# Performance work log

Measured on AMD Instinct MI355X. Metric: run time of the kernel, lower is better.

Reference implementation:

```python
import jax, jax.numpy as jnp
import numpy as np

N = 100000
E = 3200000
CONV = 16
HID = 1024
OUT = 256
NEG_SLOPE = 0.01  # torch leaky_relu default


def leaky_relu(x):
    return jnp.where(x >= 0, x, NEG_SLOPE * x)


def gcn_conv(x, W, b, src, dst, n):
    # PyG GCNConv: add self-loops, symmetric norm, linear, scatter-add, bias
    loop = jnp.arange(n)
    s = jnp.concatenate([src, loop])
    d = jnp.concatenate([dst, loop])
    deg = jax.ops.segment_sum(jnp.ones_like(d, dtype=x.dtype), d, num_segments=n)
    dinv = jnp.where(deg > 0, jax.lax.rsqrt(deg), 0.0)
    norm = dinv[s] * dinv[d]                      # [E+N]
    h = x @ W                                     # [N, out_ch]
    msg = h[s] * norm[:, None]                    # gather + scale
    out = jax.ops.segment_sum(msg, d, num_segments=n)  # scatter-add
    return out + b


def setup_inputs() -> dict:
    key = jax.random.key(0)
    ks = jax.random.split(key, 10)
    return {
        "x": jax.random.normal(ks[0], (N, 1), dtype=jnp.float32),
        "edge_index": jax.random.randint(ks[1], (2, E), 0, N, dtype=jnp.int64),
        "W1c": jax.random.normal(ks[2], (1, CONV), dtype=jnp.float32) * 0.5,
        "b1c": jnp.zeros((CONV,), dtype=jnp.float32),
        "W2c": jax.random.normal(ks[3], (CONV, 1), dtype=jnp.float32) * 0.25,
        "b2c": jnp.zeros((1,), dtype=jnp.float32),
        "Wf1": jax.random.normal(ks[4], (HID, N), dtype=jnp.float32) * 0.003,
        "bf1": jnp.zeros((HID,), dtype=jnp.float32),
        "Wf2": jax.random.normal(ks[5], (OUT, HID), dtype=jnp.float32) * 0.03,
        "bf2": jnp.zeros((OUT,), dtype=jnp.float32),
    }


def reference(x, edge_index, W1c, b1c, W2c, b2c, Wf1, bf1, Wf2, bf2):
    src, dst = edge_index[0], edge_index[1]
    h = gcn_conv(x, W1c, b1c, src, dst, N)        # [N, CONV]
    h = leaky_relu(h)
    h = gcn_conv(h, W2c, b2c, src, dst, N)        # [N, 1]
    h = leaky_relu(h)
    v = h.T.squeeze()                             # [N]
    z = leaky_relu(Wf1 @ v + bf1)                 # [HID]
    z = Wf2 @ z + bf2                             # [OUT]
    return jax.nn.log_softmax(z, axis=0)
```

## Files before the change

### kernel.cpp

```cpp
#include <hip/hip_runtime.h>
#include <math.h>


constexpr int NN    = 100000;
constexpr int NE    = 3200000;
constexpr int CONVC = 16;
constexpr int HID   = 1024;
constexpr int NOUT  = 256;
constexpr int PART  = 128;
constexpr int P     = (NN + PART - 1) / PART;
constexpr int CAP   = 5120;
constexpr int SB    = 256;
constexpr int EPB   = NE / SB;
#define NEG 0.01f

__device__ __forceinline__ float lrelu(float x) { return x >= 0.0f ? x : NEG * x; }

__device__ __forceinline__ float wave_reduce_sum(float v) {
#pragma unroll
  for (int off = 32; off > 0; off >>= 1) v += __shfl_down(v, off, 64);
  return v;
}

__global__ __launch_bounds__(256) void k_init(int* __restrict__ gcur) {
  int i = blockIdx.x * 256 + threadIdx.x;
  if (i < P) gcur[i] = i * CAP;
}

__global__ __launch_bounds__(1024) void k_bucket(const int* __restrict__ src,
                                                 const int* __restrict__ dst,
                                                 int* __restrict__ gcur,
                                                 int* __restrict__ packed) {
  __shared__ int hist[P];
  __shared__ int lcur[P];
  int t = threadIdx.x;
  for (int b = t; b < P; b += 1024) hist[b] = 0;
  __syncthreads();
  int base = blockIdx.x * EPB;
  int lim = min(EPB, NE - base);
  for (int e = t; e < lim; e += 1024) atomicAdd(&hist[dst[base + e] >> 7], 1);
  __syncthreads();
  for (int b = t; b < P; b += 1024) lcur[b] = atomicAdd(&gcur[b], hist[b]);
  __syncthreads();
  for (int e = t; e < lim; e += 1024) {
    int d = dst[base + e];
    int s = src[base + e];
    int pos = atomicAdd(&lcur[d >> 7], 1);
    packed[pos] = ((d & 127) << 17) | s;
  }
}

__global__ __launch_bounds__(256) void k_bin_deg(const int* __restrict__ packed,
                                                 const int* __restrict__ gcur,
                                                 const float* __restrict__ x,
                                                 float* __restrict__ dinv,
                                                 float* __restrict__ xs) {
  __shared__ float acc[PART];
  int p = blockIdx.x, t = threadIdx.x;
  if (t < PART) acc[t] = 0.0f;
  __syncthreads();
  int beg = p * CAP, end = gcur[p];
  for (int i = beg + t; i < end; i += 256) atomicAdd(&acc[packed[i] >> 17], 1.0f);
  __syncthreads();
  int j = p * PART + t;
  if (t < PART && j < NN) {
    float di = rsqrtf(acc[t] + 1.0f);
    dinv[j] = di;
    xs[j] = x[j] * di;
  }
}

__global__ __launch_bounds__(256) void k_bin_s1(const int* __restrict__ packed,
                                                const int* __restrict__ gcur,
                                                const float* __restrict__ val,
                                                const float* __restrict__ x,
                                                const float* __restrict__ dinv,
                                                const float* __restrict__ W1,
                                                const float* __restrict__ b1,
                                                const float* __restrict__ W2,
                                                float* __restrict__ qv,
                                                float* __restrict__ xs2) {
  __shared__ float acc[PART];
  int p = blockIdx.x, t = threadIdx.x;
  if (t < PART) acc[t] = 0.0f;
  __syncthreads();
  int beg = p * CAP, end = gcur[p];
  for (int i = beg + t; i < end; i += 256) {
    int pk = packed[i];
    atomicAdd(&acc[pk >> 17], val[pk & 0x1FFFF]);
  }
  __syncthreads();
  int j = p * PART + t;
  if (t < PART && j < NN) {
    float di = dinv[j];
    float pv = di * (acc[t] + x[j] * di);
    float q = 0.0f;
#pragma unroll
    for (int ch = 0; ch < CONVC; ch++) q += lrelu(pv * W1[ch] + b1[ch]) * W2[ch];
    qv[j] = q;
    xs2[j] = q * di;
  }
}

__global__ __launch_bounds__(256) void k_bin_s2(const int* __restrict__ packed,
                                                const int* __restrict__ gcur,
                                                const float* __restrict__ val,
                                                const float* __restrict__ qv,
                                                const float* __restrict__ dinv,
                                                const float* __restrict__ b2c,
                                                float* __restrict__ v) {
  __shared__ float acc[PART];
  int p = blockIdx.x, t = threadIdx.x;
  if (t < PART) acc[t] = 0.0f;
  __syncthreads();
  int beg = p * CAP, end = gcur[p];
  for (int i = beg + t; i < end; i += 256) {
    int pk = packed[i];
    atomicAdd(&acc[pk >> 17], val[pk & 0x1FFFF]);
  }
  __syncthreads();
  int j = p * PART + t;
  if (t < PART && j < NN) {
    float di = dinv[j];
    float r = di * (acc[t] + qv[j] * di) + b2c[0];
    v[j] = lrelu(r);
  }
}

__global__ __launch_bounds__(256) void k_mv1(const float* __restrict__ Wf1,
                                             const float* __restrict__ v,
                                             const float* __restrict__ bf1,
                                             float* __restrict__ z) {
  int row = blockIdx.x;
  const float4* w4 = reinterpret_cast<const float4*>(Wf1 + (size_t)row * NN);
  const float4* v4 = reinterpret_cast<const float4*>(v);
  float sum = 0.0f;
  for (int j = threadIdx.x; j < NN / 4; j += 256) {
    float4 w = w4[j];
    float4 vv = v4[j];
    sum += w.x * vv.x + w.y * vv.y + w.z * vv.z + w.w * vv.w;
  }
  sum = wave_reduce_sum(sum);
  __shared__ float ss[4];
  if ((threadIdx.x & 63) == 0) ss[threadIdx.x >> 6] = sum;
  __syncthreads();
  if (threadIdx.x == 0) z[row] = lrelu(ss[0] + ss[1] + ss[2] + ss[3] + bf1[row]);
}

__global__ __launch_bounds__(256) void k_mv2(const float* __restrict__ Wf2,
                                             const float* __restrict__ z,
                                             const float* __restrict__ bf2,
                                             float* __restrict__ tmp) {
  int o = blockIdx.x;
  const float4* w4 = reinterpret_cast<const float4*>(Wf2 + (size_t)o * HID);
  const float4* z4 = reinterpret_cast<const float4*>(z);
  int j = threadIdx.x;
  float4 w = w4[j];
  float4 zv = z4[j];
  float sum = w.x * zv.x + w.y * zv.y + w.z * zv.z + w.w * zv.w;
  sum = wave_reduce_sum(sum);
  __shared__ float ss[4];
  if ((threadIdx.x & 63) == 0) ss[threadIdx.x >> 6] = sum;
  __syncthreads();
  if (threadIdx.x == 0) tmp[o] = ss[0] + ss[1] + ss[2] + ss[3] + bf2[o];
}

__global__ __launch_bounds__(256) void k_lsm(const float* __restrict__ tmp,
                                             float* __restrict__ out) {
  int t = threadIdx.x;
  float vv = tmp[t];
  __shared__ float buf[256];
  buf[t] = vv;
  __syncthreads();
  for (int s = 128; s > 0; s >>= 1) {
    if (t < s) buf[t] = fmaxf(buf[t], buf[t + s]);
    __syncthreads();
  }
  float m = buf[0];
  __syncthreads();
  buf[t] = expf(vv - m);
  __syncthreads();
  for (int s = 128; s > 0; s >>= 1) {
    if (t < s) buf[t] += buf[t + s];
    __syncthreads();
  }
  float lse = logf(buf[0]);
  out[t] = vv - m - lse;
}

extern "C" void kernel_launch(void* const* d_in, const int* in_sizes, int n_in,
                              void* d_out, int out_size, void* d_ws, size_t ws_size,
                              hipStream_t stream) {
  const float* x   = (const float*)d_in[0];
  const int*   ei  = (const int*)d_in[1];
  const float* W1c = (const float*)d_in[2];
  const float* b1c = (const float*)d_in[3];
  const float* W2c = (const float*)d_in[4];
  const float* b2c = (const float*)d_in[5];
  const float* Wf1 = (const float*)d_in[6];
  const float* bf1 = (const float*)d_in[7];
  const float* Wf2 = (const float*)d_in[8];
  const float* bf2 = (const float*)d_in[9];
  float* out = (float*)d_out;

  const int* src = ei;
  const int* dst = ei + NE;

  float* ws   = (float*)d_ws;
  float* dinv = ws;
  float* xs   = dinv + NN;
  float* qv   = xs + NN;
  float* xs2  = qv + NN;
  float* v    = xs2 + NN;
  float* z    = v + NN;
  float* tmp  = z + HID;
  int*   gcur   = (int*)(tmp + NOUT);
  int*   packed = gcur + P;

  k_init<<<(P + 255) / 256, 256, 0, stream>>>(gcur);
  k_bucket<<<SB, 1024, 0, stream>>>(src, dst, gcur, packed);
  k_bin_deg<<<P, 256, 0, stream>>>(packed, gcur, x, dinv, xs);
  k_bin_s1<<<P, 256, 0, stream>>>(packed, gcur, xs, x, dinv, W1c, b1c, W2c, qv, xs2);
  k_bin_s2<<<P, 256, 0, stream>>>(packed, gcur, xs2, qv, dinv, b2c, v);
  k_mv1<<<HID, 256, 0, stream>>>(Wf1, v, bf1, z);
  k_mv2<<<NOUT, 256, 0, stream>>>(Wf2, z, bf2, tmp);
  k_lsm<<<1, 256, 0, stream>>>(tmp, out);
}
```

Baseline: 686.4 us.

## Widen bins to 256 nodes, vectorize edge loads, split shared accumulators

Bucket partitions grow from 128 to 256 destination nodes, which halves the number of bins and makes every thread in the 256-thread block own an output row. The bucketing kernel reads src and dst as int4 and keeps dst in registers between the histogram pass and the scatter pass, so dst is read from global memory only once. The per-bin kernels read packed entries as int4 and spread the shared-memory atomics over two accumulator copies to cut contention. The workspace is reordered so packed starts at the base and stays 16-byte aligned. The risks are fixed-capacity bins (CAP) that could overflow on other graphs, and more register pressure from holding dst in registers.

```diff
diff --git a/kernel.cpp b/kernel.cpp
--- a/kernel.cpp
+++ b/kernel.cpp
@@ -7,11 +7,13 @@
 constexpr int CONVC = 16;
 constexpr int HID   = 1024;
 constexpr int NOUT  = 256;
-constexpr int PART  = 128;
+constexpr int PART  = 256;
 constexpr int P     = (NN + PART - 1) / PART;
-constexpr int CAP   = 5120;
+constexpr int CAP   = 9472;
 constexpr int SB    = 256;
-constexpr int EPB   = NE / SB;
+constexpr int NE4   = NE / 4;
+constexpr int EPB4  = NE4 / SB;
+constexpr int RPT   = (EPB4 + 1023) / 1024;
 #define NEG 0.01f
 
 __device__ __forceinline__ float lrelu(float x) { return x >= 0.0f ? x : NEG * x; }
@@ -27,8 +29,8 @@
   if (i < P) gcur[i] = i * CAP;
 }
 
-__global__ __launch_bounds__(1024) void k_bucket(const int* __restrict__ src,
-                                                 const int* __restrict__ dst,
+__global__ __launch_bounds__(1024) void k_bucket(const int4* __restrict__ src4,
+                                                 const int4* __restrict__ dst4,
                                                  int* __restrict__ gcur,
                                                  int* __restrict__ packed) {
   __shared__ int hist[P];
@@ -36,17 +38,32 @@
   int t = threadIdx.x;
   for (int b = t; b < P; b += 1024) hist[b] = 0;
   __syncthreads();
-  int base = blockIdx.x * EPB;
-  int lim = min(EPB, NE - base);
-  for (int e = t; e < lim; e += 1024) atomicAdd(&hist[dst[base + e] >> 7], 1);
+  int base4 = blockIdx.x * EPB4;
+  int4 dreg[RPT];
+#pragma unroll
+  for (int k = 0; k < RPT; k++) {
+    if (t + k * 1024 < EPB4) {
+      int4 d = dst4[base4 + t + k * 1024];
+      dreg[k] = d;
+      atomicAdd(&hist[d.x >> 8], 1);
+      atomicAdd(&hist[d.y >> 8], 1);
+      atomicAdd(&hist[d.z >> 8], 1);
+      atomicAdd(&hist[d.w >> 8], 1);
+    }
+  }
   __syncthreads();
   for (int b = t; b < P; b += 1024) lcur[b] = atomicAdd(&gcur[b], hist[b]);
   __syncthreads();
-  for (int e = t; e < lim; e += 1024) {
-    int d = dst[base + e];
-    int s = src[base + e];
-    int pos = atomicAdd(&lcur[d >> 7], 1);
-    packed[pos] = ((d & 127) << 17) | s;
+#pragma unroll
+  for (int k = 0; k < RPT; k++) {
+    if (t + k * 1024 < EPB4) {
+      int4 s = src4[base4 + t + k * 1024];
+      int4 d = dreg[k];
+      int p0 = atomicAdd(&lcur[d.x >> 8], 1); packed[p0] = ((d.x & 255) << 17) | s.x;
+      int p1 = atomicAdd(&lcur[d.y >> 8], 1); packed[p1] = ((d.y & 255) << 17) | s.y;
+      int p2 = atomicAdd(&lcur[d.z >> 8], 1); packed[p2] = ((d.z & 255) << 17) | s.z;
+      int p3 = atomicAdd(&lcur[d.w >> 8], 1); packed[p3] = ((d.w & 255) << 17) | s.w;
+    }
   }
 }
 
@@ -55,16 +72,27 @@
                                                  const float* __restrict__ x,
                                                  float* __restrict__ dinv,
                                                  float* __restrict__ xs) {
-  __shared__ float acc[PART];
+  __shared__ float acc[2][PART];
   int p = blockIdx.x, t = threadIdx.x;
-  if (t < PART) acc[t] = 0.0f;
-  __syncthreads();
+  acc[0][t] = 0.0f;
+  acc[1][t] = 0.0f;
+  __syncthreads();
+  float* myacc = acc[t >> 7];
   int beg = p * CAP, end = gcur[p];
-  for (int i = beg + t; i < end; i += 256) atomicAdd(&acc[packed[i] >> 17], 1.0f);
+  int n = end - beg, n4 = n >> 2;
+  const int4* pk4 = reinterpret_cast<const int4*>(packed + beg);
+  for (int i = t; i < n4; i += 256) {
+    int4 e = pk4[i];
+    atomicAdd(&myacc[e.x >> 17], 1.0f);
+    atomicAdd(&myacc[e.y >> 17], 1.0f);
+    atomicAdd(&myacc[e.z >> 17], 1.0f);
+    atomicAdd(&myacc[e.w >> 17], 1.0f);
+  }
+  for (int i = (n4 << 2) + t; i < n; i += 256) atomicAdd(&myacc[packed[beg + i] >> 17], 1.0f);
   __syncthreads();
   int j = p * PART + t;
-  if (t < PART && j < NN) {
-    float di = rsqrtf(acc[t] + 1.0f);
+  if (j < NN) {
+    float di = rsqrtf(acc[0][t] + acc[1][t] + 1.0f);
     dinv[j] = di;
     xs[j] = x[j] * di;
   }
@@ -80,20 +108,31 @@
                                                 const float* __restrict__ W2,
                                                 float* __restrict__ qv,
                                                 float* __restrict__ xs2) {
-  __shared__ float acc[PART];
+  __shared__ float acc[2][PART];
   int p = blockIdx.x, t = threadIdx.x;
-  if (t < PART) acc[t] = 0.0f;
-  __syncthreads();
+  acc[0][t] = 0.0f;
+  acc[1][t] = 0.0f;
+  __syncthreads();
+  float* myacc = acc[t >> 7];
   int beg = p * CAP, end = gcur[p];
-  for (int i = beg + t; i < end; i += 256) {
-    int pk = packed[i];
-    atomicAdd(&acc[pk >> 17], val[pk & 0x1FFFF]);
+  int n = end - beg, n4 = n >> 2;
+  const int4* pk4 = reinterpret_cast<const int4*>(packed + beg);
+  for (int i = t; i < n4; i += 256) {
+    int4 e = pk4[i];
+    atomicAdd(&myacc[e.x >> 17], val[e.x & 0x1FFFF]);
+    atomicAdd(&myacc[e.y >> 17], val[e.y & 0x1FFFF]);
+    atomicAdd(&myacc[e.z >> 17], val[e.z & 0x1FFFF]);
+    atomicAdd(&myacc[e.w >> 17], val[e.w & 0x1FFFF]);
+  }
+  for (int i = (n4 << 2) + t; i < n; i += 256) {
+    int pk = packed[beg + i];
+    atomicAdd(&myacc[pk >> 17], val[pk & 0x1FFFF]);
   }
   __syncthreads();
   int j = p * PART + t;
-  if (t < PART && j < NN) {
+  if (j < NN) {
     float di = dinv[j];
-    float pv = di * (acc[t] + x[j] * di);
+    float pv = di * (acc[0][t] + acc[1][t] + x[j] * di);
     float q = 0.0f;
 #pragma unroll
     for (int ch = 0; ch < CONVC; ch++) q += lrelu(pv * W1[ch] + b1[ch]) * W2[ch];
@@ -109,20 +148,31 @@
                                                 const float* __restrict__ dinv,
                                                 const float* __restrict__ b2c,
                                                 float* __restrict__ v) {
-  __shared__ float acc[PART];
+  __shared__ float acc[2][PART];
   int p = blockIdx.x, t = threadIdx.x;
-  if (t < PART) acc[t] = 0.0f;
-  __syncthreads();
+  acc[0][t] = 0.0f;
+  acc[1][t] = 0.0f;
+  __syncthreads();
+  float* myacc = acc[t >> 7];
   int beg = p * CAP, end = gcur[p];
-  for (int i = beg + t; i < end; i += 256) {
-    int pk = packed[i];
-    atomicAdd(&acc[pk >> 17], val[pk & 0x1FFFF]);
+  int n = end - beg, n4 = n >> 2;
+  const int4* pk4 = reinterpret_cast<const int4*>(packed + beg);
+  for (int i = t; i < n4; i += 256) {
+    int4 e = pk4[i];
+    atomicAdd(&myacc[e.x >> 17], val[e.x & 0x1FFFF]);
+    atomicAdd(&myacc[e.y >> 17], val[e.y & 0x1FFFF]);
+    atomicAdd(&myacc[e.z >> 17], val[e.z & 0x1FFFF]);
+    atomicAdd(&myacc[e.w >> 17], val[e.w & 0x1FFFF]);
+  }
+  for (int i = (n4 << 2) + t; i < n; i += 256) {
+    int pk = packed[beg + i];
+    atomicAdd(&myacc[pk >> 17], val[pk & 0x1FFFF]);
   }
   __syncthreads();
   int j = p * PART + t;
-  if (t < PART && j < NN) {
+  if (j < NN) {
     float di = dinv[j];
-    float r = di * (acc[t] + qv[j] * di) + b2c[0];
+    float r = di * (acc[0][t] + acc[1][t] + qv[j] * di) + b2c[0];
     v[j] = lrelu(r);
   }
 }
@@ -206,19 +256,18 @@
   const int* src = ei;
   const int* dst = ei + NE;
 
-  float* ws   = (float*)d_ws;
-  float* dinv = ws;
-  float* xs   = dinv + NN;
-  float* qv   = xs + NN;
-  float* xs2  = qv + NN;
-  float* v    = xs2 + NN;
-  float* z    = v + NN;
-  float* tmp  = z + HID;
-  int*   gcur   = (int*)(tmp + NOUT);
-  int*   packed = gcur + P;
+  int*   packed = (int*)d_ws;
+  int*   gcur   = packed + (size_t)P * CAP;
+  float* dinv   = (float*)(gcur + 392);
+  float* xs     = dinv + NN;
+  float* qv     = xs + NN;
+  float* xs2    = qv + NN;
+  float* v      = xs2 + NN;
+  float* z      = v + NN;
+  float* tmp    = z + HID;
 
   k_init<<<(P + 255) / 256, 256, 0, stream>>>(gcur);
-  k_bucket<<<SB, 1024, 0, stream>>>(src, dst, gcur, packed);
+  k_bucket<<<SB, 1024, 0, stream>>>((const int4*)src, (const int4*)dst, gcur, packed);
   k_bin_deg<<<P, 256, 0, stream>>>(packed, gcur, x, dinv, xs);
   k_bin_s1<<<P, 256, 0, stream>>>(packed, gcur, xs, x, dinv, W1c, b1c, W2c, qv, xs2);
   k_bin_s2<<<P, 256, 0, stream>>>(packed, gcur, xs2, qv, dinv, b2c, v);
```

Measured after the change: 669.0 us. -2.5%, faster.
